# Optimization experiments

Measured on AMD Instinct MI355X. Metric: run time of the kernel, lower is better.

The kernel has to match this reference:

```python
import math
import jax, jax.numpy as jnp
import numpy as np

N_HEADS = 16
D_EMBED = 1024
D_HEAD = D_EMBED // N_HEADS
B, S = 4, 2048


def setup_inputs() -> dict:
    key = jax.random.key(0)
    k1, k2, k3, k4, k5 = jax.random.split(key, 5)
    scale_in = 1.0 / math.sqrt(D_EMBED)
    return {
        "x": jax.random.normal(k1, (B, S, D_EMBED), dtype=jnp.float32),
        "w_in": jax.random.normal(k2, (3 * D_EMBED, D_EMBED), dtype=jnp.float32) * scale_in,
        "b_in": jax.random.normal(k3, (3 * D_EMBED,), dtype=jnp.float32) * 0.02,
        "w_out": jax.random.normal(k4, (D_EMBED, D_EMBED), dtype=jnp.float32) * scale_in,
        "b_out": jax.random.normal(k5, (D_EMBED,), dtype=jnp.float32) * 0.02,
        "causal_mask": 1,
    }


def reference(x, w_in, b_in, w_out, b_out, causal_mask):
    Bn, Sn, D = x.shape
    # fused QKV projection (torch Linear: x @ W.T + b)
    qkv = x @ w_in.T + b_in                       # (B, S, 3D)
    q, k, v = jnp.split(qkv, 3, axis=-1)
    def to_heads(t):
        return t.reshape(Bn, Sn, N_HEADS, D_HEAD).transpose(0, 2, 1, 3)  # (B,H,S,dh)
    q, k, v = to_heads(q), to_heads(k), to_heads(v)
    # manual scaled dot-product attention, full (B,H,S,S) scores
    scores = jnp.einsum("bhqd,bhkd->bhqk", q, k)
    if causal_mask:
        tri = jnp.triu(jnp.ones((Sn, Sn), dtype=bool), k=1)
        scores = jnp.where(tri, -jnp.inf, scores)
    scores = scores / math.sqrt(D_HEAD)
    weights = jax.nn.softmax(scores, axis=-1)
    out = jnp.einsum("bhqk,bhkd->bhqd", weights, v)  # (B,H,S,dh)
    out = out.transpose(0, 2, 1, 3).reshape(Bn, Sn, D)
    return out @ w_out.T + b_out
```

## Files before the change

kernel.cpp:

```cpp
#include <hip/hip_runtime.h>

typedef __bf16 bf16x8 __attribute__((ext_vector_type(8)));
typedef float  f32x4  __attribute__((ext_vector_type(4)));
typedef unsigned int uint;

__device__ inline unsigned short f2bf(float f) {
  union { float f; unsigned int u; } v; v.f = f;
  unsigned int u = v.u;
  unsigned int r = u + 0x7FFF + ((u >> 16) & 1);
  return (unsigned short)(r >> 16);
}

__device__ inline uint pack_bf16_rhu(float a, float b) {
  uint ua = __builtin_bit_cast(uint, a) + 0x8000u;
  uint ub = __builtin_bit_cast(uint, b) + 0x8000u;
  return __builtin_amdgcn_perm(ub, ua, 0x07060302u);
}

__device__ inline void load_lds16(const unsigned short* g, unsigned short* l) {
  __builtin_amdgcn_global_load_lds(
      (const __attribute__((address_space(1))) uint*)(g),
      (__attribute__((address_space(3))) uint*)(l), 16, 0, 0);
}

__device__ inline void cvt4(const float* in, unsigned short* out) {
  float4 f = *reinterpret_cast<const float4*>(in);
  ushort4 o;
  o.x = f2bf(f.x); o.y = f2bf(f.y); o.z = f2bf(f.z); o.w = f2bf(f.w);
  *reinterpret_cast<ushort4*>(out) = o;
}

__global__ void cvt_all(const float* __restrict__ x, const float* __restrict__ w_in,
                        const float* __restrict__ w_out,
                        unsigned short* __restrict__ x_bf,
                        unsigned short* __restrict__ w_in_bf,
                        unsigned short* __restrict__ w_out_bf) {
  const int n1 = 8192 * 1024, n2 = 3072 * 1024;
  int i = (blockIdx.x * blockDim.x + threadIdx.x) * 4;
  if (i < n1)            cvt4(x + i, x_bf + i);
  else if (i < n1 + n2)  cvt4(w_in + (i - n1), w_in_bf + (i - n1));
  else                   cvt4(w_out + (i - n1 - n2), w_out_bf + (i - n1 - n2));
}

template<bool OUT_BF16, bool VSPLIT>
__global__ __launch_bounds__(256) void gemm_bt128(
    const unsigned short* __restrict__ A,
    const unsigned short* __restrict__ B,
    const float* __restrict__ bias,
    void* __restrict__ Cout,
    unsigned short* __restrict__ vt,
    int M, int N, int K, int ldc, float scale, int ncut)
{
  __shared__ __attribute__((aligned(16))) unsigned short As[128 * 64];
  __shared__ __attribute__((aligned(16))) unsigned short Bs[128 * 64];

  const int t    = threadIdx.x;
  const int wave = t >> 6, lane = t & 63;
  const int l16  = lane & 15, quad = lane >> 4;
  const int wr = wave >> 1, wc = wave & 1;
  const int m0 = blockIdx.y * 128, n0 = blockIdx.x * 128;
  const int l8 = l16 & 7;

  f32x4 acc[4][4] = {};

  for (int k0 = 0; k0 < K; k0 += 64) {
#pragma unroll
    for (int i = 0; i < 4; ++i) {
      int chunk = i * 256 + t;
      int row = chunk >> 3, cb = chunk & 7;
      int gcb = cb ^ (row & 7);
      load_lds16(A + (size_t)(m0 + row) * K + k0 + gcb * 8, As + chunk * 8);
    }
#pragma unroll
    for (int i = 0; i < 4; ++i) {
      int chunk = i * 256 + t;
      int row = chunk >> 3, cb = chunk & 7;
      int gcb = cb ^ (row & 7);
      load_lds16(B + (size_t)(n0 + row) * K + k0 + gcb * 8, Bs + chunk * 8);
    }
    __syncthreads();
#pragma unroll
    for (int ks = 0; ks < 2; ++ks) {
      bf16x8 af[4], bfr[4];
#pragma unroll
      for (int mt = 0; mt < 4; ++mt)
        af[mt] = *(const bf16x8*)(As + (wr * 64 + mt * 16 + l16) * 64 +
                                  (((ks * 4 + quad) ^ l8) << 3));
#pragma unroll
      for (int nt = 0; nt < 4; ++nt)
        bfr[nt] = *(const bf16x8*)(Bs + (wc * 64 + nt * 16 + l16) * 64 +
                                   (((ks * 4 + quad) ^ l8) << 3));
#pragma unroll
      for (int mt = 0; mt < 4; ++mt)
#pragma unroll
        for (int nt = 0; nt < 4; ++nt)
          acc[mt][nt] = __builtin_amdgcn_mfma_f32_16x16x32_bf16(af[mt], bfr[nt], acc[mt][nt], 0, 0, 0);
    }
    __syncthreads();
  }

#pragma unroll
  for (int nt = 0; nt < 4; ++nt) {
    int col = n0 + wc * 64 + nt * 16 + l16;
    float bv = bias[col];
    float mlt = (col < ncut) ? scale : 1.0f;
#pragma unroll
    for (int mt = 0; mt < 4; ++mt) {
      int row0 = m0 + wr * 64 + mt * 16 + quad * 4;
      float v0 = (acc[mt][nt][0] + bv) * mlt;
      float v1 = (acc[mt][nt][1] + bv) * mlt;
      float v2 = (acc[mt][nt][2] + bv) * mlt;
      float v3 = (acc[mt][nt][3] + bv) * mlt;
      if (VSPLIT && col >= 2048) {
        int d = col - 2048, h = d >> 6, dd = d & 63;
        int bb = row0 >> 11, s = row0 & 2047;
        uint2 w;
        w.x = pack_bf16_rhu(v0, v1);
        w.y = pack_bf16_rhu(v2, v3);
        *(uint2*)(vt + ((size_t)((bb * 16 + h) * 64 + dd) * 2048 + s)) = w;
      } else {
#pragma unroll
        for (int r = 0; r < 4; ++r) {
          float v = (r == 0) ? v0 : (r == 1) ? v1 : (r == 2) ? v2 : v3;
          if (OUT_BF16)
            ((unsigned short*)Cout)[(size_t)(row0 + r) * ldc + col] = f2bf(v);
          else
            ((float*)Cout)[(size_t)(row0 + r) * ldc + col] = v;
        }
      }
    }
  }
}

__global__ __launch_bounds__(512) void attn(
    const unsigned short* __restrict__ qkv2,
    const unsigned short* __restrict__ vt,
    unsigned short* __restrict__ y,
    const int* __restrict__ flag)
{
  __shared__ __attribute__((aligned(16))) unsigned short Qs[128 * 64];
  __shared__ __attribute__((aligned(16))) unsigned short Ks[64 * 64];
  __shared__ __attribute__((aligned(16))) unsigned short VtF[64 * 64];

  const int t    = threadIdx.x;
  const int wave = t >> 6, lane = t & 63;
  const int l16  = lane & 15, quad = lane >> 4;
  const int l8   = l16 & 7;
  const int idx = blockIdx.x;
  const int bh  = idx & 63;
  const int qt  = 15 - (idx >> 6);
  const int b = bh >> 4, h = bh & 15;
  const int causal = flag[0];
  const int q0 = qt * 128;

  const unsigned short* Qg = qkv2 + (size_t)b * 2048 * 2048 + h * 64;
  const unsigned short* Kg = Qg + 1024;
  const unsigned short* Vtg = vt + (size_t)bh * 64 * 2048;

  const int sr = t >> 2, sg = (t & 3) * 2;
  const int slot0 = sr * 64 + (((sg    ) ^ (sr & 7)) << 3);
  const int slot1 = sr * 64 + (((sg + 1) ^ (sr & 7)) << 3);
  const int kr = t >> 3, kg = t & 7;
  const int kslot = kr * 64 + ((kg ^ (kr & 7)) << 3);

  {
    const unsigned short* src = Qg + (size_t)(q0 + sr) * 2048 + sg * 8;
    *(uint4*)(Qs + slot0) = *(const uint4*)src;
    *(uint4*)(Qs + slot1) = *(const uint4*)(src + 8);
  }
  __syncthreads();
  bf16x8 qf[2];
  qf[0] = *(const bf16x8*)(Qs + (wave * 16 + l16) * 64 + (((0 + quad) ^ l8) << 3));
  qf[1] = *(const bf16x8*)(Qs + (wave * 16 + l16) * 64 + (((4 + quad) ^ l8) << 3));
  __syncthreads();
  unsigned short* Ps = Qs;

  f32x4 ot[4] = {};
  float l_lane = 0.f;
  const int q_glob = q0 + wave * 16 + l16;
  const int wq_max = q0 + wave * 16 + 15;
  const int jmax = causal ? 2 * qt + 1 : 31;

  const unsigned short* kptr = Kg + (size_t)kr * 2048 + kg * 8;
  const unsigned short* vptr = Vtg + (size_t)kr * 2048 + kg * 8;
  uint4 kreg = *(const uint4*)kptr;
  uint4 vreg = *(const uint4*)vptr;

  for (int j = 0; j <= jmax; ++j) {
    *(uint4*)(Ks + kslot)  = kreg;
    *(uint4*)(VtF + kslot) = vreg;
    __syncthreads();

    if (j < jmax) {
      kptr += 64 * 2048;
      vptr += 64;
      kreg = *(const uint4*)kptr;
      vreg = *(const uint4*)vptr;
    }

    const bool active = !causal || ((j << 6) <= wq_max);
    if (active) {
      f32x4 st[4] = {};
      __builtin_amdgcn_s_setprio(1);
#pragma unroll
      for (int ks = 0; ks < 2; ++ks) {
#pragma unroll
        for (int mt = 0; mt < 4; ++mt) {
          bf16x8 kf = *(const bf16x8*)(Ks + (mt * 16 + l16) * 64 + (((ks * 4 + quad) ^ l8) << 3));
          st[mt] = __builtin_amdgcn_mfma_f32_16x16x32_bf16(kf, qf[ks], st[mt], 0, 0, 0);
        }
      }
      __builtin_amdgcn_s_setprio(0);

      const int kv0 = j << 6;
      const bool diag = (causal != 0) && (kv0 + 63 > q_glob);
#pragma unroll
      for (int mt = 0; mt < 4; ++mt) {
        float p[4];
#pragma unroll
        for (int r = 0; r < 4; ++r) {
          float pv = __builtin_amdgcn_exp2f(st[mt][r]);
          if (diag) {
            int kv = kv0 + mt * 16 + quad * 4 + r;
            if (kv > q_glob) pv = 0.f;
          }
          p[r] = pv;
        }
        l_lane += (p[0] + p[1]) + (p[2] + p[3]);
        uint2 w;
        w.x = pack_bf16_rhu(p[0], p[1]);
        w.y = pack_bf16_rhu(p[2], p[3]);
        *(uint2*)(Ps + (wave * 16 + l16) * 64 +
                  ((((mt * 2 + (quad >> 1)) ^ l8) << 3) + (quad & 1) * 4)) = w;
      }
      __threadfence_block();

      __builtin_amdgcn_s_setprio(1);
#pragma unroll
      for (int ks = 0; ks < 2; ++ks) {
        bf16x8 pf = *(const bf16x8*)(Ps + (wave * 16 + l16) * 64 + (((ks * 4 + quad) ^ l8) << 3));
#pragma unroll
        for (int mt = 0; mt < 4; ++mt) {
          bf16x8 vf = *(const bf16x8*)(VtF + (mt * 16 + l16) * 64 + (((ks * 4 + quad) ^ l8) << 3));
          ot[mt] = __builtin_amdgcn_mfma_f32_16x16x32_bf16(vf, pf, ot[mt], 0, 0, 0);
        }
      }
      __builtin_amdgcn_s_setprio(0);
    }
    __syncthreads();
  }

  l_lane += __shfl_xor(l_lane, 16);
  l_lane += __shfl_xor(l_lane, 32);
  float inv = 1.f / l_lane;

#pragma unroll
  for (int mt = 0; mt < 4; ++mt) {
    uint2 w;
    w.x = pack_bf16_rhu(ot[mt][0] * inv, ot[mt][1] * inv);
    w.y = pack_bf16_rhu(ot[mt][2] * inv, ot[mt][3] * inv);
    *(uint2*)(Ps + (wave * 16 + l16) * 64 +
              ((((mt * 2 + (quad >> 1)) ^ l8) << 3) + (quad & 1) * 4)) = w;
  }
  __syncthreads();
  {
    size_t base = ((size_t)b * 2048 + q0 + sr) * 1024 + h * 64 + sg * 8;
    *(uint4*)(y + base)     = *(const uint4*)(Ps + slot0);
    *(uint4*)(y + base + 8) = *(const uint4*)(Ps + slot1);
  }
}

extern "C" void kernel_launch(void* const* d_in, const int* in_sizes, int n_in,
                              void* d_out, int out_size, void* d_ws, size_t ws_size,
                              hipStream_t stream) {
  const float* x     = (const float*)d_in[0];
  const float* w_in  = (const float*)d_in[1];
  const float* b_in  = (const float*)d_in[2];
  const float* w_out = (const float*)d_in[3];
  const float* b_out = (const float*)d_in[4];
  const int*   cmask = (const int*)d_in[5];

  char* ws = (char*)d_ws;
  unsigned short* x_bf     = (unsigned short*)(ws);
  unsigned short* w_in_bf  = (unsigned short*)(ws + 16777216);
  unsigned short* w_out_bf = (unsigned short*)(ws + 23068672);
  unsigned short* qkv2_bf  = (unsigned short*)(ws + 25165824);
  unsigned short* vt_bf    = (unsigned short*)(ws + 58720256);
  unsigned short* y_bf     = (unsigned short*)(ws + 75497472);

  const int ntot = (8192 + 3072 + 1024) * 1024;
  cvt_all<<<dim3(ntot / 4 / 256), 256, 0, stream>>>(x, w_in, w_out, x_bf, w_in_bf, w_out_bf);

  gemm_bt128<true, true><<<dim3(24, 64), 256, 0, stream>>>(
      x_bf, w_in_bf, b_in, qkv2_bf, vt_bf, 8192, 3072, 1024, 2048,
      0.18033688011112042f, 1024);

  attn<<<dim3(1024), 512, 0, stream>>>(qkv2_bf, vt_bf, y_bf, cmask);

  gemm_bt128<false, false><<<dim3(8, 64), 256, 0, stream>>>(
      y_bf, w_out_bf, b_out, d_out, nullptr, 8192, 1024, 1024, 1024, 1.0f, 0);
}
```

Measured before the change: 255.9 us.

## Pair causal query tiles per block and double-buffer K/V tiles in LDS

Each attention block now processes two query tiles, a long one (15-pair) and a short one (pair), so causal work per block is balanced and the grid halves to 512 blocks. K/V tiles are double-buffered in LDS, so the next tile is written while the current one is computed, leaving one barrier per iteration instead of two. This costs extra LDS, which may reduce occupancy, and runs the two halves serially inside a block.

```diff
diff --git a/kernel.cpp b/kernel.cpp
--- a/kernel.cpp
+++ b/kernel.cpp
@@ -139,22 +139,21 @@
     const int* __restrict__ flag)
 {
   __shared__ __attribute__((aligned(16))) unsigned short Qs[128 * 64];
-  __shared__ __attribute__((aligned(16))) unsigned short Ks[64 * 64];
-  __shared__ __attribute__((aligned(16))) unsigned short VtF[64 * 64];
+  __shared__ __attribute__((aligned(16))) unsigned short Ks[2][64 * 64];
+  __shared__ __attribute__((aligned(16))) unsigned short Vs[2][64 * 64];
 
   const int t    = threadIdx.x;
   const int wave = t >> 6, lane = t & 63;
   const int l16  = lane & 15, quad = lane >> 4;
   const int l8   = l16 & 7;
-  const int idx = blockIdx.x;
-  const int bh  = idx & 63;
-  const int qt  = 15 - (idx >> 6);
+  const int idx  = blockIdx.x;
+  const int bh   = idx & 63;
+  const int pair = idx >> 6;
   const int b = bh >> 4, h = bh & 15;
   const int causal = flag[0];
-  const int q0 = qt * 128;
-
-  const unsigned short* Qg = qkv2 + (size_t)b * 2048 * 2048 + h * 64;
-  const unsigned short* Kg = Qg + 1024;
+
+  const unsigned short* Qg  = qkv2 + (size_t)b * 2048 * 2048 + h * 64;
+  const unsigned short* Kg  = Qg + 1024;
   const unsigned short* Vtg = vt + (size_t)bh * 64 * 2048;
 
   const int sr = t >> 2, sg = (t & 3) * 2;
@@ -163,110 +162,130 @@
   const int kr = t >> 3, kg = t & 7;
   const int kslot = kr * 64 + ((kg ^ (kr & 7)) << 3);
 
-  {
-    const unsigned short* src = Qg + (size_t)(q0 + sr) * 2048 + sg * 8;
-    *(uint4*)(Qs + slot0) = *(const uint4*)src;
-    *(uint4*)(Qs + slot1) = *(const uint4*)(src + 8);
-  }
-  __syncthreads();
-  bf16x8 qf[2];
-  qf[0] = *(const bf16x8*)(Qs + (wave * 16 + l16) * 64 + (((0 + quad) ^ l8) << 3));
-  qf[1] = *(const bf16x8*)(Qs + (wave * 16 + l16) * 64 + (((4 + quad) ^ l8) << 3));
-  __syncthreads();
   unsigned short* Ps = Qs;
 
-  f32x4 ot[4] = {};
-  float l_lane = 0.f;
-  const int q_glob = q0 + wave * 16 + l16;
-  const int wq_max = q0 + wave * 16 + 15;
-  const int jmax = causal ? 2 * qt + 1 : 31;
-
-  const unsigned short* kptr = Kg + (size_t)kr * 2048 + kg * 8;
-  const unsigned short* vptr = Vtg + (size_t)kr * 2048 + kg * 8;
-  uint4 kreg = *(const uint4*)kptr;
-  uint4 vreg = *(const uint4*)vptr;
-
-  for (int j = 0; j <= jmax; ++j) {
-    *(uint4*)(Ks + kslot)  = kreg;
-    *(uint4*)(VtF + kslot) = vreg;
-    __syncthreads();
-
-    if (j < jmax) {
-      kptr += 64 * 2048;
-      vptr += 64;
+  for (int half = 0; half < 2; ++half) {
+    const int qt = half ? pair : (15 - pair);
+    const int q0 = qt * 128;
+    const int jmax = causal ? 2 * qt + 1 : 31;
+
+    const unsigned short* kptr = Kg + (size_t)kr * 2048 + kg * 8;
+    const unsigned short* vptr = Vtg + (size_t)kr * 2048 + kg * 8;
+    uint4 kreg = *(const uint4*)kptr;
+    uint4 vreg = *(const uint4*)vptr;
+    {
+      const unsigned short* src = Qg + (size_t)(q0 + sr) * 2048 + sg * 8;
+      *(uint4*)(Qs + slot0) = *(const uint4*)src;
+      *(uint4*)(Qs + slot1) = *(const uint4*)(src + 8);
+    }
+    __syncthreads();
+    bf16x8 qf[2];
+    qf[0] = *(const bf16x8*)(Qs + (wave * 16 + l16) * 64 + (((0 + quad) ^ l8) << 3));
+    qf[1] = *(const bf16x8*)(Qs + (wave * 16 + l16) * 64 + (((4 + quad) ^ l8) << 3));
+    __syncthreads();
+
+    *(uint4*)(Ks[0] + kslot) = kreg;
+    *(uint4*)(Vs[0] + kslot) = vreg;
+    kptr += 64 * 2048;
+    vptr += 64;
+    if (jmax > 0) {
       kreg = *(const uint4*)kptr;
       vreg = *(const uint4*)vptr;
     }
-
-    const bool active = !causal || ((j << 6) <= wq_max);
-    if (active) {
-      f32x4 st[4] = {};
-      __builtin_amdgcn_s_setprio(1);
-#pragma unroll
-      for (int ks = 0; ks < 2; ++ks) {
+    __syncthreads();
+
+    f32x4 ot[4] = {};
+    float l_lane = 0.f;
+    const int q_glob = q0 + wave * 16 + l16;
+    const int wq_max = q0 + wave * 16 + 15;
+
+    for (int j = 0; j <= jmax; ++j) {
+      const int cur = j & 1;
+      if (j < jmax) {
+        *(uint4*)(Ks[cur ^ 1] + kslot) = kreg;
+        *(uint4*)(Vs[cur ^ 1] + kslot) = vreg;
+        if (j + 1 < jmax) {
+          kptr += 64 * 2048;
+          vptr += 64;
+          kreg = *(const uint4*)kptr;
+          vreg = *(const uint4*)vptr;
+        }
+      }
+
+      const bool active = !causal || ((j << 6) <= wq_max);
+      if (active) {
+        f32x4 st[4] = {};
+        __builtin_amdgcn_s_setprio(1);
+#pragma unroll
+        for (int ks = 0; ks < 2; ++ks) {
+#pragma unroll
+          for (int mt = 0; mt < 4; ++mt) {
+            bf16x8 kf = *(const bf16x8*)(Ks[cur] + (mt * 16 + l16) * 64 +
+                                         (((ks * 4 + quad) ^ l8) << 3));
+            st[mt] = __builtin_amdgcn_mfma_f32_16x16x32_bf16(kf, qf[ks], st[mt], 0, 0, 0);
+          }
+        }
+        __builtin_amdgcn_s_setprio(0);
+
+        const int kv0 = j << 6;
+        const bool diag = (causal != 0) && (kv0 + 63 > q_glob);
 #pragma unroll
         for (int mt = 0; mt < 4; ++mt) {
-          bf16x8 kf = *(const bf16x8*)(Ks + (mt * 16 + l16) * 64 + (((ks * 4 + quad) ^ l8) << 3));
-          st[mt] = __builtin_amdgcn_mfma_f32_16x16x32_bf16(kf, qf[ks], st[mt], 0, 0, 0);
-        }
+          float p[4];
+#pragma unroll
+          for (int r = 0; r < 4; ++r) {
+            float pv = __builtin_amdgcn_exp2f(st[mt][r]);
+            if (diag) {
+              int kv = kv0 + mt * 16 + quad * 4 + r;
+              if (kv > q_glob) pv = 0.f;
+            }
+            p[r] = pv;
+          }
+          l_lane += (p[0] + p[1]) + (p[2] + p[3]);
+          uint2 w;
+          w.x = pack_bf16_rhu(p[0], p[1]);
+          w.y = pack_bf16_rhu(p[2], p[3]);
+          *(uint2*)(Ps + (wave * 16 + l16) * 64 +
+                    ((((mt * 2 + (quad >> 1)) ^ l8) << 3) + (quad & 1) * 4)) = w;
+        }
+        __threadfence_block();
+
+        __builtin_amdgcn_s_setprio(1);
+#pragma unroll
+        for (int ks = 0; ks < 2; ++ks) {
+          bf16x8 pf = *(const bf16x8*)(Ps + (wave * 16 + l16) * 64 +
+                                       (((ks * 4 + quad) ^ l8) << 3));
+#pragma unroll
+          for (int mt = 0; mt < 4; ++mt) {
+            bf16x8 vf = *(const bf16x8*)(Vs[cur] + (mt * 16 + l16) * 64 +
+                                         (((ks * 4 + quad) ^ l8) << 3));
+            ot[mt] = __builtin_amdgcn_mfma_f32_16x16x32_bf16(vf, pf, ot[mt], 0, 0, 0);
+          }
+        }
+        __builtin_amdgcn_s_setprio(0);
       }
-      __builtin_amdgcn_s_setprio(0);
-
-      const int kv0 = j << 6;
-      const bool diag = (causal != 0) && (kv0 + 63 > q_glob);
-#pragma unroll
-      for (int mt = 0; mt < 4; ++mt) {
-        float p[4];
-#pragma unroll
-        for (int r = 0; r < 4; ++r) {
-          float pv = __builtin_amdgcn_exp2f(st[mt][r]);
-          if (diag) {
-            int kv = kv0 + mt * 16 + quad * 4 + r;
-            if (kv > q_glob) pv = 0.f;
-          }
-          p[r] = pv;
-        }
-        l_lane += (p[0] + p[1]) + (p[2] + p[3]);
-        uint2 w;
-        w.x = pack_bf16_rhu(p[0], p[1]);
-        w.y = pack_bf16_rhu(p[2], p[3]);
-        *(uint2*)(Ps + (wave * 16 + l16) * 64 +
-                  ((((mt * 2 + (quad >> 1)) ^ l8) << 3) + (quad & 1) * 4)) = w;
-      }
-      __threadfence_block();
-
-      __builtin_amdgcn_s_setprio(1);
-#pragma unroll
-      for (int ks = 0; ks < 2; ++ks) {
-        bf16x8 pf = *(const bf16x8*)(Ps + (wave * 16 + l16) * 64 + (((ks * 4 + quad) ^ l8) << 3));
-#pragma unroll
-        for (int mt = 0; mt < 4; ++mt) {
-          bf16x8 vf = *(const bf16x8*)(VtF + (mt * 16 + l16) * 64 + (((ks * 4 + quad) ^ l8) << 3));
-          ot[mt] = __builtin_amdgcn_mfma_f32_16x16x32_bf16(vf, pf, ot[mt], 0, 0, 0);
-        }
-      }
-      __builtin_amdgcn_s_setprio(0);
-    }
-    __syncthreads();
-  }
-
-  l_lane += __shfl_xor(l_lane, 16);
-  l_lane += __shfl_xor(l_lane, 32);
-  float inv = 1.f / l_lane;
-
-#pragma unroll
-  for (int mt = 0; mt < 4; ++mt) {
-    uint2 w;
-    w.x = pack_bf16_rhu(ot[mt][0] * inv, ot[mt][1] * inv);
-    w.y = pack_bf16_rhu(ot[mt][2] * inv, ot[mt][3] * inv);
-    *(uint2*)(Ps + (wave * 16 + l16) * 64 +
-              ((((mt * 2 + (quad >> 1)) ^ l8) << 3) + (quad & 1) * 4)) = w;
-  }
-  __syncthreads();
-  {
-    size_t base = ((size_t)b * 2048 + q0 + sr) * 1024 + h * 64 + sg * 8;
-    *(uint4*)(y + base)     = *(const uint4*)(Ps + slot0);
-    *(uint4*)(y + base + 8) = *(const uint4*)(Ps + slot1);
+      __syncthreads();
+    }
+
+    l_lane += __shfl_xor(l_lane, 16);
+    l_lane += __shfl_xor(l_lane, 32);
+    float inv = 1.f / l_lane;
+
+#pragma unroll
+    for (int mt = 0; mt < 4; ++mt) {
+      uint2 w;
+      w.x = pack_bf16_rhu(ot[mt][0] * inv, ot[mt][1] * inv);
+      w.y = pack_bf16_rhu(ot[mt][2] * inv, ot[mt][3] * inv);
+      *(uint2*)(Ps + (wave * 16 + l16) * 64 +
+                ((((mt * 2 + (quad >> 1)) ^ l8) << 3) + (quad & 1) * 4)) = w;
+    }
+    __syncthreads();
+    {
+      size_t base = ((size_t)b * 2048 + q0 + sr) * 1024 + h * 64 + sg * 8;
+      *(uint4*)(y + base)     = *(const uint4*)(Ps + slot0);
+      *(uint4*)(y + base + 8) = *(const uint4*)(Ps + slot1);
+    }
+    __syncthreads();
   }
 }
 
@@ -295,7 +314,7 @@
       x_bf, w_in_bf, b_in, qkv2_bf, vt_bf, 8192, 3072, 1024, 2048,
       0.18033688011112042f, 1024);
 
-  attn<<<dim3(1024), 512, 0, stream>>>(qkv2_bf, vt_bf, y_bf, cmask);
+  attn<<<dim3(512), 512, 0, stream>>>(qkv2_bf, vt_bf, y_bf, cmask);
 
   gemm_bt128<false, false><<<dim3(8, 64), 256, 0, stream>>>(
       y_bf, w_out_bf, b_out, d_out, nullptr, 8192, 1024, 1024, 1024, 1.0f, 0);
```

New measurement: 241.8 us. 5.5% less time.
